# Kernel tuning notes

Measured on AMD Instinct MI355X. Metric: run time of the kernel, lower is better.

## Reference

```python
import jax, jax.numpy as jnp
import numpy as np

N0, N1, N2 = 100000, 50000, 50000
E1, E2, E12 = 1600000, 1600000, 800000
D = 128


def scatter_mean(vals, idx, size):
    # torch_scatter.scatter_mean: sum / count, 0 for empty segments
    s = jax.ops.segment_sum(vals, idx, num_segments=size)
    c = jax.ops.segment_sum(jnp.ones((vals.shape[0], 1), vals.dtype), idx, num_segments=size)
    return s / jnp.maximum(c, 1.0)


def setup_inputs() -> dict:
    key = jax.random.key(0)
    ks = jax.random.split(key, 20)
    inp = {
        "x_node": jax.random.normal(ks[0], (N0, D), jnp.float32),
        "x1": jax.random.normal(ks[1], (N1, D), jnp.float32),
        "x2": jax.random.normal(ks[2], (N2, D), jnp.float32),
        "ei1_src": jax.random.randint(ks[3], (E1,), 0, N0, jnp.int32),
        "ei1_dst": jax.random.randint(ks[4], (E1,), 0, N1, jnp.int32),
        "ei2_src": jax.random.randint(ks[5], (E2,), 0, N0, jnp.int32),
        "ei2_dst": jax.random.randint(ks[6], (E2,), 0, N2, jnp.int32),
        "ei12_src": jax.random.randint(ks[7], (E12,), 0, N1, jnp.int32),
        "ei12_dst": jax.random.randint(ks[8], (E12,), 0, N2, jnp.int32),
        "ew1": jax.random.uniform(ks[9], (E1,), jnp.float32),
        "ew2": jax.random.uniform(ks[10], (E2,), jnp.float32),
    }
    # learned params (nn.Linear: y = x @ W.T + b)
    lim = 1.0 / np.sqrt(D)
    inp["W1"] = jax.random.uniform(ks[11], (D, D), jnp.float32, -lim, lim)
    inp["b1"] = jax.random.uniform(ks[12], (D,), jnp.float32, -lim, lim)
    inp["W2"] = jax.random.uniform(ks[13], (D, D), jnp.float32, -lim, lim)
    inp["b2"] = jax.random.uniform(ks[14], (D,), jnp.float32, -lim, lim)
    inp["W12"] = jax.random.uniform(ks[15], (D, D), jnp.float32, -lim, lim)
    inp["b12"] = jax.random.uniform(ks[16], (D,), jnp.float32, -lim, lim)
    xav = np.sqrt(6.0 / (3 + D))
    inp["att_vec"] = jax.random.uniform(ks[17], (3, D), jnp.float32, -xav, xav)
    return inp


def reference(x_node, x1, x2, ei1_src, ei1_dst, ei2_src, ei2_dst,
              ei12_src, ei12_dst, ew1, ew2,
              W1, b1, W2, b2, W12, b12, att_vec):
    n0 = x_node.shape[0]
    # metapath s-1-s
    msg_1 = scatter_mean(x_node[ei1_src] * ew1[:, None], ei1_dst, x1.shape[0])
    net_msg1 = (msg_1 + x1) * 0.5
    s1s = scatter_mean(net_msg1[ei1_dst], ei1_src, n0)
    s1s = jax.nn.relu(s1s @ W1.T + b1)  # dropout: eval mode -> identity

    # metapath s-2-s
    msg_2 = scatter_mean(x_node[ei2_src] * ew2[:, None], ei2_dst, x2.shape[0])
    net_msg2 = (msg_2 + x2) * 0.5
    s2s = scatter_mean(net_msg2[ei2_dst], ei2_src, n0)
    s2s = jax.nn.relu(s2s @ W2.T + b2)

    # metapath s-1-2-s
    msg_1b = scatter_mean(x_node[ei1_src] * ew1[:, None], ei1_dst, x1.shape[0])
    net_1b = (msg_1b + x1) * 0.5
    msg_2b = scatter_mean(net_1b[ei12_src], ei12_dst, x2.shape[0])
    net_2b = (msg_2b + x2) * 0.5
    s12s = scatter_mean(net_2b[ei2_dst] * ew2[:, None], ei2_src, n0)
    s12s = jax.nn.relu(s12s @ W12.T + b12)

    all_mp = jnp.stack([s1s, s2s, s12s], axis=1)  # [N0, 3, D]
    att_scores = jnp.einsum('nkd,kd->nk', all_mp, att_vec)
    att_w = jax.nn.softmax(att_scores, axis=1)
    return jnp.einsum('nkd,nk->nd', all_mp, att_w)
```

## Files before the change

kernel.cpp:

```cpp
#include <hip/hip_runtime.h>
#include <hip/hip_fp16.h>

#define D 128
#define CAP1 80
#define CAP2 56

typedef short s16x8 __attribute__((ext_vector_type(8)));
typedef float f32x4 __attribute__((ext_vector_type(4)));

struct FillJob {
    const int* key;
    const int* other;
    const float* w;
    int* pay;
    int cbase;
    int cap;
    int E, N;
};
struct FillJobs2 { FillJob j[2]; };

__global__ __launch_bounds__(256) void fill_pair_kernel(FillJobs2 J,
                                                        int* __restrict__ cursor) {
    FillJob jb = J.j[blockIdx.y];
    int x = blockIdx.x & 7;
    int gb = blockIdx.x >> 3;
    int lo = (int)((long)jb.N * x / 8);
    int hi = (int)((long)jb.N * (x + 1) / 8);
    bool hasw = (jb.w != nullptr);
    long stride = (long)(gridDim.x >> 3) * 256;
    for (long e = (long)gb * 256 + threadIdx.x; e < jb.E; e += stride) {
        int key = jb.key[e];
        if (key < lo || key >= hi) continue;
        int pos = atomicAdd(&cursor[jb.cbase + key], 1);
        if (pos >= jb.cap) continue;
        int o = jb.other[e];
        int v;
        if (hasw) {
            int w15 = __float2int_rn(jb.w[e] * 32768.0f);
            w15 = w15 > 32767 ? 32767 : w15;
            v = (int)(((unsigned)o << 15) | (unsigned)w15);
        } else {
            v = o;
        }
        jb.pay[(long)key * jb.cap + pos] = v;
    }
}

__global__ void f2h_kernel(const float2* __restrict__ in, __half2* __restrict__ o,
                           long n2) {
    long i = (long)blockIdx.x * blockDim.x + threadIdx.x;
    if (i < n2) o[i] = __float22half2_rn(in[i]);
}

__global__ void wsplit_kernel(const float* __restrict__ W1,
                              const float* __restrict__ W2,
                              const float* __restrict__ W12,
                              unsigned short* __restrict__ hi,
                              unsigned short* __restrict__ lo) {
    int i = blockIdx.x * 256 + threadIdx.x;
    if (i >= 3 * D * D) return;
    int p = i >> 14, r = i & (D * D - 1);
    const float* W = p == 0 ? W1 : (p == 1 ? W2 : W12);
    float x = W[r];
    unsigned u = __float_as_uint(x);
    unsigned hb = u & 0xFFFF0000u;
    hi[i] = (unsigned short)(hb >> 16);
    float rem = x - __uint_as_float(hb);
    lo[i] = (unsigned short)(__float_as_uint(rem) >> 16);
}

__device__ __forceinline__ void acc8(float4 raw, float mul, float2 a[4]) {
    const __half2* h = (const __half2*)&raw;
#pragma unroll
    for (int k = 0; k < 4; ++k) {
        float2 f = __half22float2(h[k]);
        a[k].x = fmaf(f.x, mul, a[k].x);
        a[k].y = fmaf(f.y, mul, a[k].y);
    }
}

template <bool HASW>
__global__ __launch_bounds__(256) void aggh_kernel(
    const __half* __restrict__ vals, int vstride, const int* __restrict__ cnt,
    int cap, const int* __restrict__ pay, const float* __restrict__ xb,
    __half* __restrict__ dst, int dstride, int doff, int N) {
    int node = (int)(((long)blockIdx.x * 256 + threadIdx.x) >> 6);
    int lane = threadIdx.x & 63;
    if (node >= N) return;
    int count = cnt[node];
    int m = count < cap ? count : cap;
    long b0 = (long)node * cap;
    int grp = lane >> 4, il = lane & 15;
    float2 a[4] = {{0.f, 0.f}, {0.f, 0.f}, {0.f, 0.f}, {0.f, 0.f}};
    for (int base = 0; base < m; base += 64) {
        int rem = m - base;
        int n = rem < 64 ? rem : 64;
        int p = 0;
        if (lane < n) p = pay[b0 + base + lane];
        for (int j = 0; j < n; j += 4) {
            int jj = j + grp;
            int pj = __shfl(p, jj, 64);
            int g;
            float wt;
            if (HASW) {
                g = (int)(((unsigned)pj) >> 15);
                wt = (float)(pj & 0x7fff) * (1.0f / 32768.0f);
            } else {
                g = pj;
                wt = 1.0f;
            }
            float mul = jj < n ? wt : 0.0f;
            float4 raw = ((const float4*)(vals + (long)g * vstride))[il];
            acc8(raw, mul, a);
        }
    }
#pragma unroll
    for (int k = 0; k < 4; ++k) {
        a[k].x += __shfl_xor(a[k].x, 16, 64);
        a[k].y += __shfl_xor(a[k].y, 16, 64);
        a[k].x += __shfl_xor(a[k].x, 32, 64);
        a[k].y += __shfl_xor(a[k].y, 32, 64);
    }
    if (lane < 16) {
        float inv = 1.0f / fmaxf((float)count, 1.0f);
        const float4* xp = (const float4*)(xb + (long)node * D + il * 8);
        float4 x0 = xp[0], x1 = xp[1];
        float rx[8] = {x0.x, x0.y, x0.z, x0.w, x1.x, x1.y, x1.z, x1.w};
        __half2 h[4];
#pragma unroll
        for (int k = 0; k < 4; ++k) {
            float2 r;
            r.x = (a[k].x * inv + rx[2 * k + 0]) * 0.5f;
            r.y = (a[k].y * inv + rx[2 * k + 1]) * 0.5f;
            h[k] = __float22half2_rn(r);
        }
        *(float4*)(dst + (long)node * dstride + doff + il * 8) = *(float4*)h;
    }
}

__global__ __launch_bounds__(256) void aggf_kernel(
    const __half* __restrict__ vals, const int* __restrict__ cnt, int cap,
    const int* __restrict__ pay, float* __restrict__ out, int N) {
    int node = (int)(((long)blockIdx.x * 256 + threadIdx.x) >> 6);
    int lane = threadIdx.x & 63;
    if (node >= N) return;
    int count = cnt[node];
    int m = count < cap ? count : cap;
    long b0 = (long)node * cap;
    int grp = lane >> 4, il = lane & 15;
    float2 a[4] = {{0.f, 0.f}, {0.f, 0.f}, {0.f, 0.f}, {0.f, 0.f}};
    for (int base = 0; base < m; base += 64) {
        int rem = m - base;
        int n = rem < 64 ? rem : 64;
        int p = 0;
        if (lane < n) p = pay[b0 + base + lane];
        for (int j = 0; j < n; j += 4) {
            int jj = j + grp;
            int pj = __shfl(p, jj, 64);
            float mul = jj < n ? 1.0f : 0.0f;
            float4 raw = ((const float4*)(vals + (long)pj * D))[il];
            acc8(raw, mul, a);
        }
    }
#pragma unroll
    for (int k = 0; k < 4; ++k) {
        a[k].x += __shfl_xor(a[k].x, 16, 64);
        a[k].y += __shfl_xor(a[k].y, 16, 64);
        a[k].x += __shfl_xor(a[k].x, 32, 64);
        a[k].y += __shfl_xor(a[k].y, 32, 64);
    }
    if (lane < 16) {
        float inv = 1.0f / fmaxf((float)count, 1.0f);
        float4* op = (float4*)(out + (long)node * D + il * 8);
        float4 o0 = {a[0].x * inv, a[0].y * inv, a[1].x * inv, a[1].y * inv};
        float4 o1 = {a[2].x * inv, a[2].y * inv, a[3].x * inv, a[3].y * inv};
        op[0] = o0;
        op[1] = o1;
    }
}

__global__ __launch_bounds__(256) void agg2_kernel(
    const __half* __restrict__ combo, const int* __restrict__ cnt, int cap,
    const int* __restrict__ pay, float* __restrict__ outa,
    float* __restrict__ outb, int N) {
    int node = (int)(((long)blockIdx.x * 256 + threadIdx.x) >> 6);
    int lane = threadIdx.x & 63;
    if (node >= N) return;
    int count = cnt[node];
    int m = count < cap ? count : cap;
    long b0 = (long)node * cap;
    int grp = lane >> 5, il = lane & 31;
    float2 a[4] = {{0.f, 0.f}, {0.f, 0.f}, {0.f, 0.f}, {0.f, 0.f}};
    int p = 0;
    if (lane < m) p = pay[b0 + lane];
    for (int j = 0; j < m; j += 2) {
        int jj = j + grp;
        int pj = __shfl(p, jj, 64);
        int g = (int)(((unsigned)pj) >> 15);
        float w = (float)(pj & 0x7fff) * (1.0f / 32768.0f);
        float mul = jj < m ? (il < 16 ? 1.0f : w) : 0.0f;
        float4 raw = ((const float4*)(combo + (long)g * 256))[il];
        acc8(raw, mul, a);
    }
#pragma unroll
    for (int k = 0; k < 4; ++k) {
        a[k].x += __shfl_xor(a[k].x, 32, 64);
        a[k].y += __shfl_xor(a[k].y, 32, 64);
    }
    if (lane < 32) {
        float inv = 1.0f / fmaxf((float)count, 1.0f);
        float* o = (il < 16) ? (outa + (long)node * D + il * 8)
                             : (outb + (long)node * D + (il - 16) * 8);
        float4 o0 = {a[0].x * inv, a[0].y * inv, a[1].x * inv, a[1].y * inv};
        float4 o1 = {a[2].x * inv, a[2].y * inv, a[3].x * inv, a[3].y * inv};
        ((float4*)o)[0] = o0;
        ((float4*)o)[1] = o1;
    }
}

#define LO_OFF 32768

__device__ __forceinline__ int wswz(int r, int s) {
    return r * 256 + ((s ^ (r & 7)) << 4);
}

__global__ __launch_bounds__(512, 2) void mfma_tail_kernel(
    const float* __restrict__ pre1, const float* __restrict__ pre2,
    const float* pre3, const unsigned short* __restrict__ Whi,
    const unsigned short* __restrict__ Wlo, const float* __restrict__ b1,
    const float* __restrict__ b2, const float* __restrict__ b12,
    const float* __restrict__ att, float* out, int N) {
    __shared__ __align__(16) char wlds[2 * 128 * 256];
    int tid = threadIdx.x;
    int wv = tid >> 6, lane = tid & 63;
    int strip = wv >> 1, half = wv & 1;
    int rw = lane & 15, kg = lane >> 4;
    int m0 = blockIdx.x * 64 + strip * 16;
    int mrow = m0 + rw;
    if (mrow >= N) mrow = N - 1;
    const float* PRE[3] = {pre1, pre2, pre3};
    const float* BB[3] = {b1, b2, b12};

    f32x4 acc[3][4];
#pragma unroll
    for (int p = 0; p < 3; ++p)
#pragma unroll
        for (int c = 0; c < 4; ++c) acc[p][c] = (f32x4){0.f, 0.f, 0.f, 0.f};

    for (int p = 0; p < 3; ++p) {
        const unsigned short* WH = Whi + ((long)p << 14);
        const unsigned short* WL = Wlo + ((long)p << 14);
#pragma unroll
        for (int c = 0; c < 4; ++c) {
            int idx = tid + c * 512;
            int r = idx >> 4, s = idx & 15;
            int dst = wswz(r, s);
            *(float4*)(wlds + dst) = *(const float4*)(WH + r * D + s * 8);
            *(float4*)(wlds + LO_OFF + dst) =
                *(const float4*)(WL + r * D + s * 8);
        }
        __syncthreads();

        const float* src = PRE[p] + (long)mrow * D + kg * 8;
#pragma unroll
        for (int kt = 0; kt < 4; ++kt) {
            float4 xa = *(const float4*)(src + kt * 32);
            float4 xb = *(const float4*)(src + kt * 32 + 4);
            float xs[8] = {xa.x, xa.y, xa.z, xa.w, xb.x, xb.y, xb.z, xb.w};
            s16x8 ah, al;
#pragma unroll
            for (int i = 0; i < 8; ++i) {
                unsigned u = __float_as_uint(xs[i]);
                unsigned hb = u & 0xFFFF0000u;
                ah[i] = (short)(hb >> 16);
                float rem = xs[i] - __uint_as_float(hb);
                al[i] = (short)(__float_as_uint(rem) >> 16);
            }
#pragma unroll
            for (int c = 0; c < 4; ++c) {
                const char* bp =
                    wlds + wswz(half * 64 + c * 16 + rw, kt * 4 + kg);
                s16x8 bh = *(const s16x8*)bp;
                s16x8 bl = *(const s16x8*)(bp + LO_OFF);
                acc[p][c] = __builtin_amdgcn_mfma_f32_16x16x32_bf16(
                    ah, bh, acc[p][c], 0, 0, 0);
                acc[p][c] = __builtin_amdgcn_mfma_f32_16x16x32_bf16(
                    ah, bl, acc[p][c], 0, 0, 0);
                acc[p][c] = __builtin_amdgcn_mfma_f32_16x16x32_bf16(
                    al, bh, acc[p][c], 0, 0, 0);
            }
        }
        __syncthreads();
    }

    float sc[3][4] = {{0.f, 0.f, 0.f, 0.f},
                      {0.f, 0.f, 0.f, 0.f},
                      {0.f, 0.f, 0.f, 0.f}};
#pragma unroll
    for (int p = 0; p < 3; ++p) {
#pragma unroll
        for (int c = 0; c < 4; ++c) {
            int col = half * 64 + c * 16 + rw;
            float bv = BB[p][col];
            float av = att[p * D + col];
#pragma unroll
            for (int j = 0; j < 4; ++j) {
                float v = fmaxf(acc[p][c][j] + bv, 0.0f);
                acc[p][c][j] = v;
                sc[p][j] = fmaf(v, av, sc[p][j]);
            }
        }
    }
#pragma unroll
    for (int j = 0; j < 4; ++j) {
#pragma unroll
        for (int off = 1; off < 16; off <<= 1) {
            sc[0][j] += __shfl_xor(sc[0][j], off, 64);
            sc[1][j] += __shfl_xor(sc[1][j], off, 64);
            sc[2][j] += __shfl_xor(sc[2][j], off, 64);
        }
    }
    float* sred = (float*)wlds;
    if (rw == 0) {
#pragma unroll
        for (int p = 0; p < 3; ++p)
#pragma unroll
            for (int j = 0; j < 4; ++j)
                sred[((strip * 2 + half) * 3 + p) * 16 + kg * 4 + j] = sc[p][j];
    }
    __syncthreads();

#pragma unroll
    for (int j = 0; j < 4; ++j) {
        int row = kg * 4 + j;
        float s0 = sred[((strip * 2 + 0) * 3 + 0) * 16 + row] +
                   sred[((strip * 2 + 1) * 3 + 0) * 16 + row];
        float s1 = sred[((strip * 2 + 0) * 3 + 1) * 16 + row] +
                   sred[((strip * 2 + 1) * 3 + 1) * 16 + row];
        float s2 = sred[((strip * 2 + 0) * 3 + 2) * 16 + row] +
                   sred[((strip * 2 + 1) * 3 + 2) * 16 + row];
        float mx = fmaxf(s0, fmaxf(s1, s2));
        float e0 = __expf(s0 - mx), e1 = __expf(s1 - mx), e2 = __expf(s2 - mx);
        float inv = 1.0f / (e0 + e1 + e2);
        float w0 = e0 * inv, w1 = e1 * inv, w2 = e2 * inv;
        int orow = m0 + row;
        if (orow < N) {
            long ro = (long)orow * D + half * 64 + rw;
#pragma unroll
            for (int c = 0; c < 4; ++c) {
                out[ro + c * 16] =
                    acc[0][c][j] * w0 + acc[1][c][j] * w1 + acc[2][c][j] * w2;
            }
        }
    }
}

extern "C" void kernel_launch(void* const* d_in, const int* in_sizes, int n_in,
                              void* d_out, int out_size, void* d_ws,
                              size_t ws_size, hipStream_t stream) {
    const float* x_node = (const float*)d_in[0];
    const float* x1 = (const float*)d_in[1];
    const float* x2 = (const float*)d_in[2];
    const int* ei1_src = (const int*)d_in[3];
    const int* ei1_dst = (const int*)d_in[4];
    const int* ei2_src = (const int*)d_in[5];
    const int* ei2_dst = (const int*)d_in[6];
    const int* ei12_src = (const int*)d_in[7];
    const int* ei12_dst = (const int*)d_in[8];
    const float* ew1 = (const float*)d_in[9];
    const float* ew2 = (const float*)d_in[10];
    const float* W1 = (const float*)d_in[11];
    const float* b1 = (const float*)d_in[12];
    const float* W2 = (const float*)d_in[13];
    const float* b2 = (const float*)d_in[14];
    const float* W12 = (const float*)d_in[15];
    const float* b12 = (const float*)d_in[16];
    const float* att = (const float*)d_in[17];
    float* out = (float*)d_out;

    const int N0 = in_sizes[0] / D;
    const int N1 = in_sizes[1] / D;
    const int N2 = in_sizes[2] / D;
    const int E1 = in_sizes[3];
    const int E2 = in_sizes[5];
    const int E12 = in_sizes[7];

    float* ws = (float*)d_ws;
    size_t off = 0;
    auto A = [](size_t v) { return (v + 3) & ~(size_t)3; };

    __half* xh = (__half*)(ws + off);    off += A((size_t)N0 * D / 2);
    __half* net1h = (__half*)(ws + off); off += A((size_t)N1 * D / 2);
    __half* combo = (__half*)(ws + off); off += A((size_t)N2 * D);

    size_t pA = off;
    int* pay_d12 = (int*)(ws + off); off += A((size_t)N2 * CAP2);
    int* pay_s1 = (int*)(ws + off);  off += A((size_t)N0 * CAP2);
    size_t needA = pA + (size_t)N0 * D;
    if (off < needA) off = needA;
    float* pre2 = ws + pA;

    size_t pB = off;
    int* pay_d1 = (int*)(ws + off); off += A((size_t)N1 * CAP1);
    int* pay_d2 = (int*)(ws + off); off += A((size_t)N2 * CAP1);
    size_t needB = pB + (size_t)N0 * D;
    if (off < needB) off = needB;
    float* pre1 = ws + pB;

    int* pay_s2 = (int*)(ws + off); off += A((size_t)N0 * CAP2);
    float* pre3 = out;

    unsigned short* Whi = (unsigned short*)(ws + off); off += A((size_t)3 * D * D / 2);
    unsigned short* Wlo = (unsigned short*)(ws + off); off += A((size_t)3 * D * D / 2);

    const int NT = N1 + 2 * N2 + 2 * N0;
    int* cur = (int*)(ws + off); off += A(NT);
    const int cb_d1 = 0, cb_d2 = N1, cb_d12 = N1 + N2;
    const int cb_s1 = N1 + 2 * N2, cb_s2 = N1 + 2 * N2 + N0;

    hipMemsetAsync((void*)cur, 0, (size_t)NT * sizeof(int), stream);

    long n2 = (long)N0 * D / 2;
    f2h_kernel<<<(n2 + 255) / 256, 256, 0, stream>>>((const float2*)x_node,
                                                     (__half2*)xh, n2);
    wsplit_kernel<<<(3 * D * D + 255) / 256, 256, 0, stream>>>(W1, W2, W12,
                                                               Whi, Wlo);

    FillJob jd1 = {ei1_dst, ei1_src, ew1, pay_d1, cb_d1, CAP1, E1, N1};
    FillJob jd2 = {ei2_dst, ei2_src, ew2, pay_d2, cb_d2, CAP1, E2, N2};
    FillJob jd12 = {ei12_dst, ei12_src, nullptr, pay_d12, cb_d12, CAP2, E12, N2};
    FillJob js1 = {ei1_src, ei1_dst, nullptr, pay_s1, cb_s1, CAP2, E1, N0};
    FillJob js2 = {ei2_src, ei2_dst, ew2, pay_s2, cb_s2, CAP2, E2, N0};
    FillJobs2 P1 = {{jd1, jd2}};
    FillJobs2 P2 = {{jd12, js1}};
    FillJobs2 P3 = {{js2, js2}};
    fill_pair_kernel<<<dim3(4096, 2), 256, 0, stream>>>(P1, cur);
    fill_pair_kernel<<<dim3(4096, 2), 256, 0, stream>>>(P2, cur);
    fill_pair_kernel<<<dim3(4096, 1), 256, 0, stream>>>(P3, cur);

    auto blocks = [](int n) { return (n + 3) / 4; };
    aggh_kernel<true><<<blocks(N1), 256, 0, stream>>>(
        xh, D, cur + cb_d1, CAP1, pay_d1, x1, net1h, D, 0, N1);
    aggh_kernel<true><<<blocks(N2), 256, 0, stream>>>(
        xh, D, cur + cb_d2, CAP1, pay_d2, x2, combo, 2 * D, 0, N2);
    aggh_kernel<false><<<blocks(N2), 256, 0, stream>>>(
        net1h, D, cur + cb_d12, CAP2, pay_d12, x2, combo, 2 * D, D, N2);
    aggf_kernel<<<blocks(N0), 256, 0, stream>>>(net1h, cur + cb_s1, CAP2,
                                                pay_s1, pre1, N0);
    agg2_kernel<<<blocks(N0), 256, 0, stream>>>(combo, cur + cb_s2, CAP2,
                                                pay_s2, pre2, pre3, N0);

    mfma_tail_kernel<<<(N0 + 63) / 64, 512, 0, stream>>>(
        pre1, pre2, pre3, Whi, Wlo, b1, b2, b12, att, out, N0);
}
```

Measured before the change: 892.6 us.

## Replace 8-way filtered edge scan with two-pass octant binning then scatter

The previous fill kernel made every edge be read by each of 8 key-range partitions, so every edge array was scanned eight times. The new code first bins edges into 8 key-octant buckets with wave-level prefix sums and one atomic per wave per octant, writing (key, payload) records. A second kernel then scatters each octant's records into per-node slots. This cuts the repeated edge reads but adds an intermediate record buffer, reused from the net1h/combo workspace region, plus six launches in place of three.

```diff
diff --git a/kernel.cpp b/kernel.cpp
--- a/kernel.cpp
+++ b/kernel.cpp
@@ -8,41 +8,122 @@
 typedef short s16x8 __attribute__((ext_vector_type(8)));
 typedef float f32x4 __attribute__((ext_vector_type(4)));
 
-struct FillJob {
+struct BinJob {
     const int* key;
     const int* other;
     const float* w;
+    int2* rec;
+    int* bcur;
+    float oscale;
+    int capo;
+    int E;
+};
+struct BinJobs2 { BinJob j[2]; };
+
+struct ScatJob {
+    const int2* rec;
+    const int* bcur;
     int* pay;
     int cbase;
     int cap;
-    int E, N;
+    int capo;
 };
-struct FillJobs2 { FillJob j[2]; };
-
-__global__ __launch_bounds__(256) void fill_pair_kernel(FillJobs2 J,
-                                                        int* __restrict__ cursor) {
-    FillJob jb = J.j[blockIdx.y];
-    int x = blockIdx.x & 7;
+struct ScatJobs2 { ScatJob j[2]; };
+
+__device__ __forceinline__ int packpay(int o, float w) {
+    int w15 = __float2int_rn(w * 32768.0f);
+    w15 = w15 > 32767 ? 32767 : w15;
+    return (int)(((unsigned)o << 15) | (unsigned)w15);
+}
+
+__global__ __launch_bounds__(256) void bin_kernel(BinJobs2 J) {
+    BinJob jb = J.j[blockIdx.y];
+    bool hasw = (jb.w != nullptr);
+    int tid = threadIdx.x;
+    int wv = tid >> 6, lane = tid & 63;
+    long E = jb.E;
+    for (long cb = (long)blockIdx.x * 4096; cb < E;
+         cb += (long)gridDim.x * 4096) {
+        long wb = cb + (long)wv * 1024;
+        if (wb >= E) continue;
+        long eb = wb + (long)lane * 16;
+        int key[16], oct[16], v[16];
+        if (wb + 1024 <= E) {
+#pragma unroll
+            for (int q = 0; q < 4; ++q) {
+                int4 kk = *(const int4*)(jb.key + eb + q * 4);
+                int4 oo = *(const int4*)(jb.other + eb + q * 4);
+                key[q * 4 + 0] = kk.x; key[q * 4 + 1] = kk.y;
+                key[q * 4 + 2] = kk.z; key[q * 4 + 3] = kk.w;
+                if (hasw) {
+                    float4 ww = *(const float4*)(jb.w + eb + q * 4);
+                    v[q * 4 + 0] = packpay(oo.x, ww.x);
+                    v[q * 4 + 1] = packpay(oo.y, ww.y);
+                    v[q * 4 + 2] = packpay(oo.z, ww.z);
+                    v[q * 4 + 3] = packpay(oo.w, ww.w);
+                } else {
+                    v[q * 4 + 0] = oo.x; v[q * 4 + 1] = oo.y;
+                    v[q * 4 + 2] = oo.z; v[q * 4 + 3] = oo.w;
+                }
+            }
+        } else {
+#pragma unroll
+            for (int i = 0; i < 16; ++i) {
+                long e = eb + i;
+                if (e < E) {
+                    key[i] = jb.key[e];
+                    int o = jb.other[e];
+                    v[i] = hasw ? packpay(o, jb.w[e]) : o;
+                } else {
+                    key[i] = -1;
+                }
+            }
+        }
+#pragma unroll
+        for (int i = 0; i < 16; ++i) {
+            int oc = (int)((float)key[i] * jb.oscale);
+            oct[i] = (key[i] < 0) ? -1 : (oc > 7 ? 7 : oc);
+        }
+        for (int o = 0; o < 8; ++o) {
+            int cnt = 0;
+#pragma unroll
+            for (int i = 0; i < 16; ++i) cnt += (oct[i] == o);
+            int incl = cnt;
+            for (int d = 1; d < 64; d <<= 1) {
+                int t = __shfl_up(incl, d, 64);
+                if (lane >= d) incl += t;
+            }
+            int total = __shfl(incl, 63, 64);
+            if (total == 0) continue;
+            int base = 0;
+            if (lane == 63) base = atomicAdd(jb.bcur + o, total);
+            base = __shfl(base, 63, 64);
+            int s = base + incl - cnt;
+            int2* seg = jb.rec + (long)o * jb.capo;
+#pragma unroll
+            for (int i = 0; i < 16; ++i) {
+                if (oct[i] == o) {
+                    if (s < jb.capo) seg[s] = make_int2(key[i], v[i]);
+                    ++s;
+                }
+            }
+        }
+    }
+}
+
+__global__ __launch_bounds__(256) void scat_kernel(ScatJobs2 J,
+                                                   int* __restrict__ cursor) {
+    ScatJob jb = J.j[blockIdx.y];
+    int o = blockIdx.x & 7;
     int gb = blockIdx.x >> 3;
-    int lo = (int)((long)jb.N * x / 8);
-    int hi = (int)((long)jb.N * (x + 1) / 8);
-    bool hasw = (jb.w != nullptr);
+    int cnt = jb.bcur[o];
+    if (cnt > jb.capo) cnt = jb.capo;
+    const int2* seg = jb.rec + (long)o * jb.capo;
     long stride = (long)(gridDim.x >> 3) * 256;
-    for (long e = (long)gb * 256 + threadIdx.x; e < jb.E; e += stride) {
-        int key = jb.key[e];
-        if (key < lo || key >= hi) continue;
-        int pos = atomicAdd(&cursor[jb.cbase + key], 1);
-        if (pos >= jb.cap) continue;
-        int o = jb.other[e];
-        int v;
-        if (hasw) {
-            int w15 = __float2int_rn(jb.w[e] * 32768.0f);
-            w15 = w15 > 32767 ? 32767 : w15;
-            v = (int)(((unsigned)o << 15) | (unsigned)w15);
-        } else {
-            v = o;
-        }
-        jb.pay[(long)key * jb.cap + pos] = v;
+    for (long i = (long)gb * 256 + threadIdx.x; i < cnt; i += stride) {
+        int2 r = seg[i];
+        int pos = atomicAdd(&cursor[jb.cbase + r.x], 1);
+        if (pos < jb.cap) jb.pay[(long)r.x * jb.cap + pos] = r.y;
     }
 }
 
@@ -390,6 +471,7 @@
     auto A = [](size_t v) { return (v + 3) & ~(size_t)3; };
 
     __half* xh = (__half*)(ws + off);    off += A((size_t)N0 * D / 2);
+    size_t off_net = off;
     __half* net1h = (__half*)(ws + off); off += A((size_t)N1 * D / 2);
     __half* combo = (__half*)(ws + off); off += A((size_t)N2 * D);
 
@@ -414,11 +496,12 @@
     unsigned short* Wlo = (unsigned short*)(ws + off); off += A((size_t)3 * D * D / 2);
 
     const int NT = N1 + 2 * N2 + 2 * N0;
-    int* cur = (int*)(ws + off); off += A(NT);
+    int* cur = (int*)(ws + off); off += A(NT + 40);
+    int* bcur = cur + NT;
     const int cb_d1 = 0, cb_d2 = N1, cb_d12 = N1 + N2;
     const int cb_s1 = N1 + 2 * N2, cb_s2 = N1 + 2 * N2 + N0;
 
-    hipMemsetAsync((void*)cur, 0, (size_t)NT * sizeof(int), stream);
+    hipMemsetAsync((void*)cur, 0, (size_t)(NT + 40) * sizeof(int), stream);
 
     long n2 = (long)N0 * D / 2;
     f2h_kernel<<<(n2 + 255) / 256, 256, 0, stream>>>((const float2*)x_node,
@@ -426,17 +509,35 @@
     wsplit_kernel<<<(3 * D * D + 255) / 256, 256, 0, stream>>>(W1, W2, W12,
                                                                Whi, Wlo);
 
-    FillJob jd1 = {ei1_dst, ei1_src, ew1, pay_d1, cb_d1, CAP1, E1, N1};
-    FillJob jd2 = {ei2_dst, ei2_src, ew2, pay_d2, cb_d2, CAP1, E2, N2};
-    FillJob jd12 = {ei12_dst, ei12_src, nullptr, pay_d12, cb_d12, CAP2, E12, N2};
-    FillJob js1 = {ei1_src, ei1_dst, nullptr, pay_s1, cb_s1, CAP2, E1, N0};
-    FillJob js2 = {ei2_src, ei2_dst, ew2, pay_s2, cb_s2, CAP2, E2, N0};
-    FillJobs2 P1 = {{jd1, jd2}};
-    FillJobs2 P2 = {{jd12, js1}};
-    FillJobs2 P3 = {{js2, js2}};
-    fill_pair_kernel<<<dim3(4096, 2), 256, 0, stream>>>(P1, cur);
-    fill_pair_kernel<<<dim3(4096, 2), 256, 0, stream>>>(P2, cur);
-    fill_pair_kernel<<<dim3(4096, 1), 256, 0, stream>>>(P3, cur);
+    auto capof = [](int E) { return E / 8 + E / 32 + 1024; };
+    int capo1 = capof(E1), capo2 = capof(E2), capo12 = capof(E12);
+    int2* recA = (int2*)(ws + off_net);
+    int2* rec_d12 = recA + (size_t)8 * capo1;
+    BinJob bd1 = {ei1_dst, ei1_src, ew1, recA, bcur + 0, 8.0f / N1, capo1, E1};
+    BinJob bd12 = {ei12_dst, ei12_src, nullptr, rec_d12, bcur + 8,
+                   8.0f / N2, capo12, E12};
+    BinJobs2 B1 = {{bd1, bd12}};
+    bin_kernel<<<dim3(1024, 2), 256, 0, stream>>>(B1);
+    ScatJob sd1 = {recA, bcur + 0, pay_d1, cb_d1, CAP1, capo1};
+    ScatJob sd12 = {rec_d12, bcur + 8, pay_d12, cb_d12, CAP2, capo12};
+    ScatJobs2 S1 = {{sd1, sd12}};
+    scat_kernel<<<dim3(4096, 2), 256, 0, stream>>>(S1, cur);
+    int2* rec_s1 = recA + (size_t)8 * capo2;
+    BinJob bd2 = {ei2_dst, ei2_src, ew2, recA, bcur + 16, 8.0f / N2, capo2, E2};
+    BinJob bs1 = {ei1_src, ei1_dst, nullptr, rec_s1, bcur + 24,
+                  8.0f / N0, capo1, E1};
+    BinJobs2 B2 = {{bd2, bs1}};
+    bin_kernel<<<dim3(1024, 2), 256, 0, stream>>>(B2);
+    ScatJob sd2 = {recA, bcur + 16, pay_d2, cb_d2, CAP1, capo2};
+    ScatJob ss1 = {rec_s1, bcur + 24, pay_s1, cb_s1, CAP2, capo1};
+    ScatJobs2 S2 = {{sd2, ss1}};
+    scat_kernel<<<dim3(4096, 2), 256, 0, stream>>>(S2, cur);
+    BinJob bs2 = {ei2_src, ei2_dst, ew2, recA, bcur + 32, 8.0f / N0, capo2, E2};
+    BinJobs2 B3 = {{bs2, bs2}};
+    bin_kernel<<<dim3(1024, 1), 256, 0, stream>>>(B3);
+    ScatJob ss2 = {recA, bcur + 32, pay_s2, cb_s2, CAP2, capo2};
+    ScatJobs2 S3 = {{ss2, ss2}};
+    scat_kernel<<<dim3(4096, 1), 256, 0, stream>>>(S3, cur);
 
     auto blocks = [](int n) { return (n + 3) / 4; };
     aggh_kernel<true><<<blocks(N1), 256, 0, stream>>>(
```

After: 1.538 ms. 72.3% more time.

## Replace filtered edge fill with two-pass binning by key octant then scatter

Applied to the files above, without the earlier changes.

The old fill kernel had every block read all edges and keep only those whose key fell in its octant, so the edge arrays were read eight times. The new path has a bin kernel read each edge once and write (key, payload) records into per-block, per-octant buckets using shared-memory atomics. A scatter kernel then walks each octant's buckets and does the global cursor atomics with better key locality. This adds ten launches instead of three and an intermediate record buffer placed over the net1h/combo workspace. Bucket capacity is fixed, so edges beyond it are silently dropped if keys are skewed.

```diff
diff --git a/kernel.cpp b/kernel.cpp
--- a/kernel.cpp
+++ b/kernel.cpp
@@ -4,45 +4,78 @@
 #define D 128
 #define CAP1 80
 #define CAP2 56
+#define NBLK 1024
 
 typedef short s16x8 __attribute__((ext_vector_type(8)));
 typedef float f32x4 __attribute__((ext_vector_type(4)));
 
-struct FillJob {
+struct BinJob {
     const int* key;
     const int* other;
     const float* w;
+    int2* rec;
+    int* bcur;
+    float oscale;
+    int capb;
+    int E;
+    int per;
+};
+
+struct ScatJob {
+    const int2* rec;
+    const int* bcur;
     int* pay;
     int cbase;
     int cap;
-    int E, N;
+    int capb;
 };
-struct FillJobs2 { FillJob j[2]; };
-
-__global__ __launch_bounds__(256) void fill_pair_kernel(FillJobs2 J,
-                                                        int* __restrict__ cursor) {
-    FillJob jb = J.j[blockIdx.y];
-    int x = blockIdx.x & 7;
+
+__device__ __forceinline__ int packpay(int o, float w) {
+    int w15 = __float2int_rn(w * 32768.0f);
+    w15 = w15 > 32767 ? 32767 : w15;
+    return (int)(((unsigned)o << 15) | (unsigned)w15);
+}
+
+__global__ __launch_bounds__(256) void bin_kernel(BinJob jb) {
+    __shared__ int lcur[8];
+    int tid = threadIdx.x;
+    if (tid < 8) lcur[tid] = 0;
+    __syncthreads();
+    long lo = (long)blockIdx.x * jb.per;
+    long hi = lo + jb.per;
+    if (hi > jb.E) hi = jb.E;
+    bool hasw = (jb.w != nullptr);
+    int2* myrec = jb.rec + (long)blockIdx.x * 8 * jb.capb;
+    for (long e = lo + tid; e < hi; e += 256) {
+        int k = jb.key[e];
+        int o = jb.other[e];
+        int v = hasw ? packpay(o, jb.w[e]) : o;
+        int oc = (int)((float)k * jb.oscale);
+        oc = oc > 7 ? 7 : oc;
+        int pos = atomicAdd(&lcur[oc], 1);
+        if (pos < jb.capb) myrec[oc * jb.capb + pos] = make_int2(k, v);
+    }
+    __syncthreads();
+    if (tid < 8) {
+        int c = lcur[tid];
+        jb.bcur[blockIdx.x * 8 + tid] = c < jb.capb ? c : jb.capb;
+    }
+}
+
+__global__ __launch_bounds__(256) void scat_kernel(ScatJob jb,
+                                                   int* __restrict__ cursor) {
+    int o = blockIdx.x & 7;
     int gb = blockIdx.x >> 3;
-    int lo = (int)((long)jb.N * x / 8);
-    int hi = (int)((long)jb.N * (x + 1) / 8);
-    bool hasw = (jb.w != nullptr);
-    long stride = (long)(gridDim.x >> 3) * 256;
-    for (long e = (long)gb * 256 + threadIdx.x; e < jb.E; e += stride) {
-        int key = jb.key[e];
-        if (key < lo || key >= hi) continue;
-        int pos = atomicAdd(&cursor[jb.cbase + key], 1);
-        if (pos >= jb.cap) continue;
-        int o = jb.other[e];
-        int v;
-        if (hasw) {
-            int w15 = __float2int_rn(jb.w[e] * 32768.0f);
-            w15 = w15 > 32767 ? 32767 : w15;
-            v = (int)(((unsigned)o << 15) | (unsigned)w15);
-        } else {
-            v = o;
-        }
-        jb.pay[(long)key * jb.cap + pos] = v;
+    int nb = gridDim.x >> 3;
+    int tid = threadIdx.x;
+    for (int b = gb; b < NBLK; b += nb) {
+        int cnt = jb.bcur[b * 8 + o];
+        const int2* seg = jb.rec + ((long)b * 8 + o) * jb.capb;
+        for (int i = tid; i < cnt; i += 256) {
+            int2 r = seg[i];
+            int pos = atomicAdd(&cursor[jb.cbase + r.x], 1);
+            if (pos < jb.cap) jb.pay[(long)r.x * jb.cap + pos] = r.y;
+        }
     }
 }
 
@@ -390,6 +423,7 @@
     auto A = [](size_t v) { return (v + 3) & ~(size_t)3; };
 
     __half* xh = (__half*)(ws + off);    off += A((size_t)N0 * D / 2);
+    size_t off_net = off;
     __half* net1h = (__half*)(ws + off); off += A((size_t)N1 * D / 2);
     __half* combo = (__half*)(ws + off); off += A((size_t)N2 * D);
 
@@ -415,6 +449,7 @@
 
     const int NT = N1 + 2 * N2 + 2 * N0;
     int* cur = (int*)(ws + off); off += A(NT);
+    int* bcur = (int*)(ws + off); off += A((size_t)NBLK * 8);
     const int cb_d1 = 0, cb_d2 = N1, cb_d12 = N1 + N2;
     const int cb_s1 = N1 + 2 * N2, cb_s2 = N1 + 2 * N2 + N0;
 
@@ -426,17 +461,26 @@
     wsplit_kernel<<<(3 * D * D + 255) / 256, 256, 0, stream>>>(W1, W2, W12,
                                                                Whi, Wlo);
 
-    FillJob jd1 = {ei1_dst, ei1_src, ew1, pay_d1, cb_d1, CAP1, E1, N1};
-    FillJob jd2 = {ei2_dst, ei2_src, ew2, pay_d2, cb_d2, CAP1, E2, N2};
-    FillJob jd12 = {ei12_dst, ei12_src, nullptr, pay_d12, cb_d12, CAP2, E12, N2};
-    FillJob js1 = {ei1_src, ei1_dst, nullptr, pay_s1, cb_s1, CAP2, E1, N0};
-    FillJob js2 = {ei2_src, ei2_dst, ew2, pay_s2, cb_s2, CAP2, E2, N0};
-    FillJobs2 P1 = {{jd1, jd2}};
-    FillJobs2 P2 = {{jd12, js1}};
-    FillJobs2 P3 = {{js2, js2}};
-    fill_pair_kernel<<<dim3(4096, 2), 256, 0, stream>>>(P1, cur);
-    fill_pair_kernel<<<dim3(4096, 2), 256, 0, stream>>>(P2, cur);
-    fill_pair_kernel<<<dim3(4096, 1), 256, 0, stream>>>(P3, cur);
+    int2* rec = (int2*)(ws + off_net);
+    struct JobDesc {
+        const int* key; const int* other; const float* w;
+        int* pay; int cbase; int cap; int E; int N;
+    } JD[5] = {
+        {ei1_dst, ei1_src, ew1, pay_d1, cb_d1, CAP1, E1, N1},
+        {ei2_dst, ei2_src, ew2, pay_d2, cb_d2, CAP1, E2, N2},
+        {ei12_dst, ei12_src, nullptr, pay_d12, cb_d12, CAP2, E12, N2},
+        {ei1_src, ei1_dst, nullptr, pay_s1, cb_s1, CAP2, E1, N0},
+        {ei2_src, ei2_dst, ew2, pay_s2, cb_s2, CAP2, E2, N0},
+    };
+    for (int j = 0; j < 5; ++j) {
+        int per = (JD[j].E + NBLK - 1) / NBLK;
+        int capb = per / 8 + per / 16 + 64;
+        BinJob bj = {JD[j].key, JD[j].other, JD[j].w, rec, bcur,
+                     8.0f / JD[j].N, capb, JD[j].E, per};
+        bin_kernel<<<NBLK, 256, 0, stream>>>(bj);
+        ScatJob sj = {rec, bcur, JD[j].pay, JD[j].cbase, JD[j].cap, capb};
+        scat_kernel<<<4096, 256, 0, stream>>>(sj, cur);
+    }
 
     auto blocks = [](int n) { return (n + 3) / 4; };
     aggh_kernel<true><<<blocks(N1), 256, 0, stream>>>(
```

Measured after the change: 918.1 us. 1.03x slower.
